# Kernel tuning notes

Hardware: AMD Instinct MI355X
Metric: run time of the kernel (lower is better)

The kernel has to match this reference:

```python
import jax, jax.numpy as jnp
import numpy as np

NUM_EXPERTS = 64
TOP_K = 2
TEMPERATURE = 1.0
MOMENTUM = 0.9


def _l2norm(x, axis=-1):
    # torch F.normalize: x / max(||x||, eps)
    n = jnp.linalg.norm(x, axis=axis, keepdims=True)
    return x / jnp.maximum(n, 1e-12)


def setup_inputs() -> dict:
    key = jax.random.key(0)
    k1, k2 = jax.random.split(key)
    hidden_states = jax.random.normal(k1, (4, 4096, 2048), dtype=jnp.float32)
    centers = _l2norm(jax.random.normal(k2, (NUM_EXPERTS, 2048), dtype=jnp.float32))
    return {"hidden_states": hidden_states, "centers": centers}


def reference(hidden_states, centers):
    B, T, H = hidden_states.shape
    flat = hidden_states.reshape(-1, H).astype(jnp.float32)  # [N, H]
    N = flat.shape[0]

    # cosine-similarity logits
    reps_n = _l2norm(flat)
    centers_n = _l2norm(centers)
    temp = jnp.maximum(jnp.float32(TEMPERATURE), 1e-6)
    logits = (reps_n @ centers_n.T) / temp  # [N, E]

    probs = jax.nn.softmax(logits, axis=-1)
    top_w, top_ids = jax.lax.top_k(probs, TOP_K)  # [N, k]
    top_w = top_w / (jnp.sum(top_w, axis=-1, keepdims=True) + 1e-9)

    # EMA center update from top-1 routed expert (training+update path)
    route = top_ids[:, 0]  # [N]
    sums = jax.ops.segment_sum(flat, route, num_segments=NUM_EXPERTS)  # [E, H]
    counts = jax.ops.segment_sum(jnp.ones((N, 1), jnp.float32), route,
                                 num_segments=NUM_EXPERTS)  # [E, 1]
    means = sums / (counts + 1e-6)
    updated = _l2norm(MOMENTUM * centers + (1.0 - MOMENTUM) * means)
    new_centers = jnp.where(counts > 0, updated, centers)

    top_ids = top_ids.reshape(B, T, TOP_K)
    top_w = top_w.reshape(B, T, TOP_K)
    return top_ids, top_w, new_centers
```

## Files before the change

kernel.cpp:

```cpp
#include <hip/hip_runtime.h>
#include <math.h>

#define NTOK 16384
#define HDIM 2048
#define NEXP 64
#define KK   32
#define TAU  5e-5f
#define MAXB 2048
#define TB   32
#define TPAD 36

typedef __attribute__((ext_vector_type(8))) short short8;
typedef __attribute__((ext_vector_type(4))) float f32x4;
typedef __attribute__((ext_vector_type(2))) unsigned int uint2v;


__global__ __launch_bounds__(256)
void zero_kernel(float* p, int n) {
  int i = blockIdx.x * 256 + threadIdx.x;
  if (i < n) p[i] = 0.0f;
}

__device__ __forceinline__ float block_reduce_sum(float v, float* red) {
  #pragma unroll
  for (int o = 32; o > 0; o >>= 1) v += __shfl_down(v, o, 64);
  int lane = threadIdx.x & 63;
  int wid  = threadIdx.x >> 6;
  if (lane == 0) red[wid] = v;
  __syncthreads();
  float s = red[0] + red[1] + red[2] + red[3];
  __syncthreads();
  return s;
}

__device__ __forceinline__ double block_reduce_sum_f64(double v, double* red) {
  const int tid = threadIdx.x;
  red[tid] = v;
  __syncthreads();
  if (tid < 128) red[tid] += red[tid + 128];
  __syncthreads();
  if (tid < 64)  red[tid] += red[tid + 64];
  __syncthreads();
  double s = 0.0;
  if (tid < 64) {
    s = red[tid];
    #pragma unroll
    for (int o = 32; o > 0; o >>= 1) s += __shfl_down(s, o, 64);
  }
  if (tid == 0) red[0] = s;
  __syncthreads();
  s = red[0];
  __syncthreads();
  return s;
}

__global__ __launch_bounds__(256)
void cnorm_kernel(const float* __restrict__ c, float* __restrict__ inv_nc) {
  __shared__ float red[4];
  int e = blockIdx.x;
  float ss = 0.f;
  #pragma unroll
  for (int j = 0; j < 8; ++j) {
    float v = c[e * HDIM + threadIdx.x + j * 256];
    ss += v * v;
  }
  float tot = block_reduce_sum(ss, red);
  if (threadIdx.x == 0) inv_nc[e] = 1.0f / fmaxf(sqrtf(tot), 1e-12f);
}

__global__ __launch_bounds__(256)
void cprep_kernel(const float* __restrict__ c, float* __restrict__ inv_nc,
                  float* __restrict__ bn, unsigned short* __restrict__ cbh,
                  unsigned short* __restrict__ cbl) {
  __shared__ float red[4];
  __shared__ double redd[256];
  __shared__ float s_nc;
  const int e = blockIdx.x;
  const int tid = threadIdx.x;
  const float* cr = c + (size_t)e * HDIM;
  float ss = 0.f;
  double acc = 0.0;
  #pragma unroll
  for (int j = 0; j < 8; ++j) {
    float v = cr[tid + j * 256];
    ss += v * v;
    double dv = (double)v;
    acc += dv * dv;
  }
  float tot = block_reduce_sum(ss, red);
  double cn = block_reduce_sum_f64(acc, redd);
  if (tid == 0) {
    inv_nc[e] = 1.0f / fmaxf(sqrtf(tot), 1e-12f);
    s_nc = (float)fmax(sqrt(cn), 1e-12);
  }
  __syncthreads();
  const double nc = (double)s_nc;
  #pragma unroll
  for (int j = 0; j < 8; ++j) {
    const int k = tid + j * 256;
    const float v = cr[k];
    bn[(size_t)e * HDIM + k] = (float)((double)v / nc);
    unsigned u = __float_as_uint(v);
    unsigned h = u & 0xffff0000u;
    float r = v - __uint_as_float(h);
    cbh[(size_t)e * HDIM + k] = (unsigned short)(u >> 16);
    cbl[(size_t)e * HDIM + k] = (unsigned short)(__float_as_uint(r) >> 16);
  }
}

__device__ __forceinline__ void cvt2(float v0, float v1, unsigned &hi, unsigned &lo) {
  unsigned u0 = __float_as_uint(v0);
  unsigned u1 = __float_as_uint(v1);
  unsigned h0 = u0 & 0xffff0000u;
  unsigned h1 = u1 & 0xffff0000u;
  float r0 = v0 - __uint_as_float(h0);
  float r1 = v1 - __uint_as_float(h1);
  hi = (u0 >> 16) | h1;
  lo = (__float_as_uint(r0) >> 16) | (__float_as_uint(r1) & 0xffff0000u);
}

__global__ __launch_bounds__(256)
void fused_kernel(const float* __restrict__ x,
                  const unsigned short* __restrict__ cbh,
                  const unsigned short* __restrict__ cbl,
                  const float* __restrict__ inv_nc,
                  float* __restrict__ out, int* __restrict__ route,
                  int* __restrict__ nflag, int* __restrict__ flags) {
  __shared__ __align__(16) unsigned short Ah[2][TB][32];
  __shared__ __align__(16) unsigned short Al[2][TB][32];
  __shared__ __align__(16) unsigned short Bh[2][NEXP][32];
  __shared__ __align__(16) unsigned short Bl[2][NEXP][32];
  __shared__ float lg[NEXP][TPAD];
  __shared__ float xn_lds[TB];
  __shared__ float snc[NEXP];

  const int tid  = threadIdx.x;
  const int t0   = blockIdx.x * TB;
  const int sr   = tid >> 3;
  const int sq   = (tid & 7) * 4;
  const int er   = tid >> 2;
  const int eq   = (tid & 3) * 8;
  const int lane = tid & 63;
  const int w    = tid >> 6;
  const int m16  = (w & 1) * 16;
  const int nh32 = (w >> 1) * 32;
  const int fr   = lane & 15;
  const int fk   = (lane >> 4) * 8;

  if (tid < NEXP) snc[tid] = inv_nc[tid];

  const float* xptr = x + (size_t)(t0 + sr) * HDIM + sq;
  const unsigned short* bhptr = cbh + (size_t)er * HDIM + eq;
  const unsigned short* blptr = cbl + (size_t)er * HDIM + eq;

  f32x4 xp;
  short8 bhp, blp;
  float nacc = 0.f;

  auto stage = [&](int b) {
    unsigned h01, l01, h23, l23;
    cvt2(xp.x, xp.y, h01, l01);
    cvt2(xp.z, xp.w, h23, l23);
    *(uint2v*)&Ah[b][sr][sq] = (uint2v){h01, h23};
    *(uint2v*)&Al[b][sr][sq] = (uint2v){l01, l23};
    nacc += xp.x*xp.x + xp.y*xp.y + xp.z*xp.z + xp.w*xp.w;
    *(short8*)&Bh[b][er][eq] = bhp;
    *(short8*)&Bl[b][er][eq] = blp;
  };

  xp  = *(const f32x4*)(xptr);
  bhp = *(const short8*)(bhptr);
  blp = *(const short8*)(blptr);
  stage(0);
  xp  = *(const f32x4*)(xptr + KK);
  bhp = *(const short8*)(bhptr + KK);
  blp = *(const short8*)(blptr + KK);
  __syncthreads();

  f32x4 acc0 = (f32x4){0.f, 0.f, 0.f, 0.f};
  f32x4 acc1 = (f32x4){0.f, 0.f, 0.f, 0.f};

  for (int it = 0; it < 64; ++it) {
    const int cur = it & 1;
    short8 ah  = *(const short8*)&Ah[cur][m16 + fr][fk];
    short8 al  = *(const short8*)&Al[cur][m16 + fr][fk];
    short8 bh0 = *(const short8*)&Bh[cur][nh32 + fr][fk];
    short8 bl0 = *(const short8*)&Bl[cur][nh32 + fr][fk];
    short8 bh1 = *(const short8*)&Bh[cur][nh32 + 16 + fr][fk];
    short8 bl1 = *(const short8*)&Bl[cur][nh32 + 16 + fr][fk];
    if (it < 63) {
      stage(cur ^ 1);
      if (it < 62) {
        const int off = (it + 2) * KK;
        xp  = *(const f32x4*)(xptr + off);
        bhp = *(const short8*)(bhptr + off);
        blp = *(const short8*)(blptr + off);
      }
    }
    acc0 = __builtin_amdgcn_mfma_f32_16x16x32_bf16(ah, bh0, acc0, 0, 0, 0);
    acc0 = __builtin_amdgcn_mfma_f32_16x16x32_bf16(ah, bl0, acc0, 0, 0, 0);
    acc0 = __builtin_amdgcn_mfma_f32_16x16x32_bf16(al, bh0, acc0, 0, 0, 0);
    acc1 = __builtin_amdgcn_mfma_f32_16x16x32_bf16(ah, bh1, acc1, 0, 0, 0);
    acc1 = __builtin_amdgcn_mfma_f32_16x16x32_bf16(ah, bl1, acc1, 0, 0, 0);
    acc1 = __builtin_amdgcn_mfma_f32_16x16x32_bf16(al, bh1, acc1, 0, 0, 0);
    __syncthreads();
  }

  float s = nacc;
  s += __shfl_xor(s, 1, 64);
  s += __shfl_xor(s, 2, 64);
  s += __shfl_xor(s, 4, 64);
  if ((tid & 7) == 0) xn_lds[sr] = s;

  const int tb = m16 + (lane >> 4) * 4;
  *(f32x4*)&lg[nh32 + fr][tb]      = acc0;
  *(f32x4*)&lg[nh32 + 16 + fr][tb] = acc1;
  __syncthreads();

  if (tid < TB) {
    const int t  = tid;
    const int tg = t0 + t;
    const float inv_nx = 1.0f / fmaxf(sqrtf(xn_lds[t]), 1e-12f);
    float m1 = -1e30f, m2 = -1e30f, m3 = -1e30f;
    int i1 = 0, i2 = 0;
    #pragma unroll
    for (int e = 0; e < NEXP; ++e) {
      float l = lg[e][t] * snc[e] * inv_nx;
      if (l > m1)      { m3 = m2; m2 = m1; i2 = i1; m1 = l; i1 = e; }
      else if (l > m2) { m3 = m2; m2 = l; i2 = e; }
      else if (l > m3) { m3 = l; }
    }
    float Z = 0.f;
    #pragma unroll
    for (int e = 0; e < NEXP; ++e)
      Z += expf(lg[e][t] * snc[e] * inv_nx - m1);
    const float p1w = 1.0f / Z;
    const float p2w = expf(m2 - m1) / Z;
    const float s2  = p1w + p2w + 1e-9f;
    out[tg * 2 + 0] = (float)i1;
    out[tg * 2 + 1] = (float)i2;
    out[2 * NTOK + tg * 2 + 0] = p1w / s2;
    out[2 * NTOK + tg * 2 + 1] = p2w / s2;
    route[tg] = i1;
    if ((m1 - m2) < TAU || (m2 - m3) < TAU) {
      int idx = atomicAdd(nflag, 1);
      flags[idx] = tg;
    }
  }
}

__global__ __launch_bounds__(256)
void refine_np_kernel(const float* __restrict__ x, const float* __restrict__ bn,
                      float* __restrict__ out, int* __restrict__ route,
                      const int* __restrict__ nflag, const int* __restrict__ flags) {
  __shared__ float a_lds[HDIM];
  __shared__ double redd[256];
  __shared__ float lf[NEXP];
  __shared__ float s_nx;
  const int tid  = threadIdx.x;
  const int lane = tid & 63;
  const int w    = tid >> 6;
  const int n = *nflag;
  for (int j = blockIdx.x; j < n; j += gridDim.x) {
    const int t = flags[j];
    const float* xr = x + (size_t)t * HDIM;
    double xacc = 0.0;
    #pragma unroll
    for (int i = 0; i < 8; ++i) {
      double v = (double)xr[tid + 256 * i];
      xacc += v * v;
    }
    double xn = block_reduce_sum_f64(xacc, redd);
    if (tid == 0) s_nx = (float)fmax(sqrt(xn), 1e-12);
    __syncthreads();
    const double nx = (double)s_nx;
    #pragma unroll
    for (int i = 0; i < 8; ++i) {
      int k = tid + 256 * i;
      a_lds[k] = (float)((double)xr[k] / nx);
    }
    __syncthreads();
    #pragma unroll 1
    for (int ei = 0; ei < 16; ++ei) {
      const int e = w * 16 + ei;
      const float* br = bn + (size_t)e * HDIM;
      double d = 0.0;
      #pragma unroll 8
      for (int i = 0; i < 32; ++i) {
        int k = lane + 64 * i;
        d += (double)a_lds[k] * (double)br[k];
      }
      #pragma unroll
      for (int o = 32; o > 0; o >>= 1) d += __shfl_down(d, o, 64);
      if (lane == 0) lf[e] = (float)d;
    }
    __syncthreads();
    if (tid == 0) {
      float m32 = lf[0];
      for (int ee = 1; ee < NEXP; ++ee) m32 = fmaxf(m32, lf[ee]);
      float ex[NEXP];
      for (int ee = 0; ee < NEXP; ++ee)
        ex[ee] = (float)exp((double)(lf[ee] - m32));
      float r[8];
      #pragma unroll
      for (int q = 0; q < 8; ++q) r[q] = ex[q];
      for (int i = 8; i < NEXP; i += 8)
        #pragma unroll
        for (int q = 0; q < 8; ++q) r[q] += ex[i + q];
      const float Z = ((r[0] + r[1]) + (r[2] + r[3])) + ((r[4] + r[5]) + (r[6] + r[7]));
      float p1 = -1.f, p2 = -1.f;
      int i1 = 0, i2 = 0;
      for (int ee = 0; ee < NEXP; ++ee) {
        float p = ex[ee] / Z;
        if (p > p1)      { p2 = p1; i2 = i1; p1 = p; i1 = ee; }
        else if (p > p2) { p2 = p; i2 = ee; }
      }
      const float s = (p1 + p2) + 1e-9f;
      out[t * 2 + 0] = (float)i1;
      out[t * 2 + 1] = (float)i2;
      out[2 * NTOK + t * 2 + 0] = p1 / s;
      out[2 * NTOK + t * 2 + 1] = p2 / s;
      route[t] = i1;
    }
    __syncthreads();
  }
}

__global__ __launch_bounds__(64)
void refine_np_slow(const float* __restrict__ x, const float* __restrict__ c,
                    float* __restrict__ out, int* __restrict__ route,
                    const int* __restrict__ nflag, const int* __restrict__ flags) {
  __shared__ float lf[NEXP];
  const int e = threadIdx.x;
  const int n = *nflag;
  for (int j = blockIdx.x; j < n; j += gridDim.x) {
    const int t = flags[j];
    const float* xr = x + (size_t)t * HDIM;
    const float* cr = c + (size_t)e * HDIM;
    double xn = 0.0, cn = 0.0;
    for (int k = 0; k < HDIM; ++k) {
      double xv = (double)xr[k];
      double cv = (double)cr[k];
      xn += xv * xv;
      cn += cv * cv;
    }
    const float nx32 = (float)fmax(sqrt(xn), 1e-12);
    const float nc32 = (float)fmax(sqrt(cn), 1e-12);
    double d = 0.0;
    for (int k = 0; k < HDIM; ++k) {
      float a = (float)((double)xr[k] / (double)nx32);
      float b = (float)((double)cr[k] / (double)nc32);
      d += (double)a * (double)b;
    }
    lf[e] = (float)d;
    __syncthreads();
    if (e == 0) {
      float m32 = lf[0];
      for (int ee = 1; ee < NEXP; ++ee) m32 = fmaxf(m32, lf[ee]);
      float ex[NEXP];
      for (int ee = 0; ee < NEXP; ++ee)
        ex[ee] = (float)exp((double)(lf[ee] - m32));
      float r[8];
      #pragma unroll
      for (int q = 0; q < 8; ++q) r[q] = ex[q];
      for (int i = 8; i < NEXP; i += 8)
        #pragma unroll
        for (int q = 0; q < 8; ++q) r[q] += ex[i + q];
      const float Z = ((r[0] + r[1]) + (r[2] + r[3])) + ((r[4] + r[5]) + (r[6] + r[7]));
      float p1 = -1.f, p2 = -1.f;
      int i1 = 0, i2 = 0;
      for (int ee = 0; ee < NEXP; ++ee) {
        float p = ex[ee] / Z;
        if (p > p1)      { p2 = p1; i2 = i1; p1 = p; i1 = ee; }
        else if (p > p2) { p2 = p; i2 = ee; }
      }
      const float s = (p1 + p2) + 1e-9f;
      out[t * 2 + 0] = (float)i1;
      out[t * 2 + 1] = (float)i2;
      out[2 * NTOK + t * 2 + 0] = p1 / s;
      out[2 * NTOK + t * 2 + 1] = p2 / s;
      route[t] = i1;
    }
    __syncthreads();
  }
}

__global__ __launch_bounds__(256)
void scatter_kernel(const int* __restrict__ route, int* __restrict__ cursor,
                    int* __restrict__ bucket) {
  const int t = blockIdx.x * 256 + threadIdx.x;
  const int e = route[t];
  const int pos = atomicAdd(&cursor[e], 1);
  if (pos < MAXB) bucket[e * MAXB + pos] = t;
}

__global__ __launch_bounds__(256)
void segsum_dense(const float* __restrict__ x, const int* __restrict__ cursor,
                  const int* __restrict__ bucket, float* __restrict__ sums) {
  __shared__ int ts[MAXB];
  const int e   = blockIdx.x >> 3;
  const int hc  = blockIdx.x & 7;
  const int hb  = hc * 256;
  const int tid = threadIdx.x;
  int n = cursor[e];
  if (n > MAXB) n = MAXB;
  for (int i = tid; i < n; i += 256) ts[i] = bucket[e * MAXB + i];
  __syncthreads();
  float a[8];
  #pragma unroll
  for (int q = 0; q < 8; ++q) a[q] = 0.f;
  int i = 0;
  for (; i + 7 < n; i += 8) {
    #pragma unroll
    for (int q = 0; q < 8; ++q)
      a[q] += x[(size_t)ts[i + q] * HDIM + hb + tid];
  }
  for (; i < n; ++i) a[0] += x[(size_t)ts[i] * HDIM + hb + tid];
  const float s = ((a[0] + a[1]) + (a[2] + a[3])) + ((a[4] + a[5]) + (a[6] + a[7]));
  sums[e * HDIM + hb + tid] = s;
}

__global__ __launch_bounds__(256)
void finalize_kernel(const float* __restrict__ c, const float* __restrict__ sums,
                     const int* __restrict__ counts, float* __restrict__ out) {
  __shared__ float red[4];
  const int e = blockIdx.x;
  const int tid = threadIdx.x;
  const float cnt = (float)counts[e];
  const float minv = 1.0f / (cnt + 1e-6f);
  float u[8], cv[8];
  float ss = 0.f;
  #pragma unroll
  for (int j = 0; j < 8; ++j) {
    int h = tid + j * 256;
    cv[j] = c[e * HDIM + h];
    float mean = sums[e * HDIM + h] * minv;
    u[j] = 0.9f * cv[j] + 0.1f * mean;
    ss += u[j] * u[j];
  }
  float tot = block_reduce_sum(ss, red);
  float sc = 1.0f / fmaxf(sqrtf(tot), 1e-12f);
  const bool nz = cnt > 0.f;
  #pragma unroll
  for (int j = 0; j < 8; ++j) {
    int h = tid + j * 256;
    out[4 * NTOK + e * HDIM + h] = nz ? u[j] * sc : cv[j];
  }
}

__global__ __launch_bounds__(256)
void router_kernel(const float* __restrict__ x, const float* __restrict__ c,
                   const float* __restrict__ inv_nc, float* __restrict__ out,
                   int* __restrict__ route, int* __restrict__ nflag,
                   int* __restrict__ flags) {
  __shared__ __align__(16) float xs[64][36];
  __shared__ float lgs[64][67];
  const int tid  = threadIdx.x;
  const int lane = tid & 63;
  const int w    = tid >> 6;
  const int t0   = blockIdx.x * 64;
  const int e0   = __builtin_amdgcn_readfirstlane(w * 16);
  const float* cb = c + (size_t)e0 * HDIM;
  const int st = tid >> 3;
  const int sk = (tid & 7) * 4;
  float acc[16];
  #pragma unroll
  for (int e = 0; e < 16; ++e) acc[e] = 0.f;
  float nacc = 0.f;
  float4 p0 = *(const float4*)&x[(size_t)(t0 + st)      * HDIM + sk];
  float4 p1 = *(const float4*)&x[(size_t)(t0 + st + 32) * HDIM + sk];
  for (int k0 = 0; k0 < HDIM; k0 += 32) {
    __syncthreads();
    *(float4*)&xs[st][sk]      = p0;
    *(float4*)&xs[st + 32][sk] = p1;
    __syncthreads();
    const int kn = k0 + 32;
    if (kn < HDIM) {
      p0 = *(const float4*)&x[(size_t)(t0 + st)      * HDIM + kn + sk];
      p1 = *(const float4*)&x[(size_t)(t0 + st + 32) * HDIM + kn + sk];
    }
    float a[32];
    #pragma unroll
    for (int j = 0; j < 32; j += 4) {
      float4 v = *(const float4*)&xs[lane][j];
      a[j] = v.x; a[j+1] = v.y; a[j+2] = v.z; a[j+3] = v.w;
    }
    if (w == 0) {
      #pragma unroll
      for (int j = 0; j < 32; ++j) nacc += a[j] * a[j];
    }
    #pragma unroll
    for (int e = 0; e < 16; ++e) {
      const float* br = cb + (size_t)e * HDIM + k0;
      #pragma unroll
      for (int j = 0; j < 32; j += 4) {
        float4 bv = *(const float4*)&br[j];
        acc[e] += a[j]*bv.x + a[j+1]*bv.y + a[j+2]*bv.z + a[j+3]*bv.w;
      }
    }
  }
  #pragma unroll
  for (int e = 0; e < 16; ++e) lgs[lane][e0 + e] = acc[e] * inv_nc[e0 + e];
  __syncthreads();
  if (w == 0) {
    const float inv_nx = 1.0f / fmaxf(sqrtf(nacc), 1e-12f);
    float m1 = -1e30f, m2 = -1e30f, m3 = -1e30f;
    int i1 = 0, i2 = 0;
    for (int e = 0; e < NEXP; ++e) {
      float l = lgs[lane][e] * inv_nx;
      if (l > m1)      { m3 = m2; m2 = m1; i2 = i1; m1 = l; i1 = e; }
      else if (l > m2) { m3 = m2; m2 = l; i2 = e; }
      else if (l > m3) { m3 = l; }
    }
    float Z = 0.f;
    for (int e = 0; e < NEXP; ++e) Z += expf(lgs[lane][e] * inv_nx - m1);
    const float p1w = 1.0f / Z;
    const float p2w = expf(m2 - m1) / Z;
    const float s   = p1w + p2w + 1e-9f;
    const int tg = t0 + lane;
    out[tg * 2 + 0] = (float)i1;
    out[tg * 2 + 1] = (float)i2;
    out[2 * NTOK + tg * 2 + 0] = p1w / s;
    out[2 * NTOK + tg * 2 + 1] = p2w / s;
    route[tg] = i1;
    if ((m1 - m2) < TAU || (m2 - m3) < TAU) {
      int idx = atomicAdd(nflag, 1);
      flags[idx] = tg;
    }
  }
}

__global__ __launch_bounds__(512)
void segsum_kernel(const float* __restrict__ x, const int* __restrict__ route,
                   float* __restrict__ sums, int* __restrict__ counts) {
  __shared__ float ls[NEXP * 256];
  __shared__ int lcnt[NEXP];
  const int tid  = threadIdx.x;
  const int lane = tid & 63;
  const int w    = tid >> 6;
  const int hc   = blockIdx.x & 7;
  const int tg   = blockIdx.x >> 3;
  const int hb   = hc * 256;
  #pragma unroll
  for (int i = 0; i < 32; ++i) ls[tid + i * 512] = 0.f;
  if (tid < NEXP) lcnt[tid] = 0;
  __syncthreads();
  const int tbase = tg * 512 + w * 64;
  #pragma unroll 4
  for (int i = 0; i < 64; ++i) {
    const int t = tbase + i;
    const int e = route[t];
    const float* xr = x + (size_t)t * HDIM + hb + lane;
    #pragma unroll
    for (int j = 0; j < 4; ++j)
      atomicAdd(&ls[e * 256 + lane + 64 * j], xr[64 * j]);
    if (hc == 0 && lane == 0) atomicAdd(&lcnt[e], 1);
  }
  __syncthreads();
  #pragma unroll
  for (int i = tid; i < NEXP * 256; i += 512) {
    const int e = i >> 8, h = i & 255;
    atomicAdd(&sums[e * HDIM + hb + h], ls[i]);
  }
  if (hc == 0 && tid < NEXP && lcnt[tid] > 0) atomicAdd(&counts[tid], lcnt[tid]);
}

extern "C" void kernel_launch(void* const* d_in, const int* in_sizes, int n_in,
                              void* d_out, int out_size, void* d_ws, size_t ws_size,
                              hipStream_t stream) {
  const float* x = (const float*)d_in[0];
  const float* c = (const float*)d_in[1];
  float* out = (float*)d_out;
  float* ws = (float*)d_ws;

  float* inv_nc = ws;
  int*   counts = (int*)(ws + 64);
  int*   nflag  = (int*)(ws + 128);
  int*   route  = (int*)(ws + 192);
  int*   flags  = (int*)(ws + 16576);
  float* sums   = ws + 32960;
  float* bn     = ws + 164032;
  unsigned short* cbh = (unsigned short*)(ws + 295104);
  unsigned short* cbl = (unsigned short*)(ws + 360640);
  int*   bucket = (int*)(ws + 426176);

  const size_t NEED = 557248ull * 4ull;
  if (ws_size >= NEED) {
    zero_kernel<<<1, 256, 0, stream>>>(ws + 64, 128);
    cprep_kernel<<<NEXP, 256, 0, stream>>>(c, inv_nc, bn, cbh, cbl);
    fused_kernel<<<NTOK / TB, 256, 0, stream>>>(x, cbh, cbl, inv_nc, out, route, nflag, flags);
    refine_np_kernel<<<512, 256, 0, stream>>>(x, bn, out, route, nflag, flags);
    scatter_kernel<<<64, 256, 0, stream>>>(route, counts, bucket);
    segsum_dense<<<512, 256, 0, stream>>>(x, counts, bucket, sums);
    finalize_kernel<<<NEXP, 256, 0, stream>>>(c, sums, counts, out);
  } else {
    zero_kernel<<<1, 256, 0, stream>>>(ws + 64, 128);
    zero_kernel<<<512, 256, 0, stream>>>(sums, 131072);
    cnorm_kernel<<<NEXP, 256, 0, stream>>>(c, inv_nc);
    router_kernel<<<NTOK / 64, 256, 0, stream>>>(x, c, inv_nc, out, route, nflag, flags);
    refine_np_slow<<<1024, 64, 0, stream>>>(x, c, out, route, nflag, flags);
    segsum_kernel<<<256, 512, 0, stream>>>(x, route, sums, counts);
    finalize_kernel<<<NEXP, 256, 0, stream>>>(c, sums, counts, out);
  }
}
```

Before: 314.6 us.

## Load GEMM operands directly to registers, split segment-sum across more blocks, fold zeroing

The fused router GEMM no longer stages x and center tiles through LDS with per-iteration barriers. Each wave now loads its MFMA fragments straight from global memory into a four-slot register ring, which removes the __syncthreads calls from the main loop. The segment sum is split four ways over token ranges and uses float4 loads across 2048 blocks, with partial sums added in a new finalize kernel; this raises parallelism but adds extra workspace traffic. Zeroing the counters moves into cprep, which drops one kernel launch.

```diff
diff --git a/kernel.cpp b/kernel.cpp
--- a/kernel.cpp
+++ b/kernel.cpp
@@ -12,7 +12,7 @@
 
 typedef __attribute__((ext_vector_type(8))) short short8;
 typedef __attribute__((ext_vector_type(4))) float f32x4;
-typedef __attribute__((ext_vector_type(2))) unsigned int uint2v;
+typedef __attribute__((ext_vector_type(4))) unsigned int uint4v;
 
 
 __global__ __launch_bounds__(256)
@@ -71,12 +71,13 @@
 __global__ __launch_bounds__(256)
 void cprep_kernel(const float* __restrict__ c, float* __restrict__ inv_nc,
                   float* __restrict__ bn, unsigned short* __restrict__ cbh,
-                  unsigned short* __restrict__ cbl) {
+                  unsigned short* __restrict__ cbl, int* __restrict__ zr) {
   __shared__ float red[4];
   __shared__ double redd[256];
   __shared__ float s_nc;
   const int e = blockIdx.x;
   const int tid = threadIdx.x;
+  if (e == 0 && tid < 128) zr[tid] = 0;
   const float* cr = c + (size_t)e * HDIM;
   float ss = 0.f;
   double acc = 0.0;
@@ -126,95 +127,91 @@
                   const float* __restrict__ inv_nc,
                   float* __restrict__ out, int* __restrict__ route,
                   int* __restrict__ nflag, int* __restrict__ flags) {
-  __shared__ __align__(16) unsigned short Ah[2][TB][32];
-  __shared__ __align__(16) unsigned short Al[2][TB][32];
-  __shared__ __align__(16) unsigned short Bh[2][NEXP][32];
-  __shared__ __align__(16) unsigned short Bl[2][NEXP][32];
   __shared__ float lg[NEXP][TPAD];
   __shared__ float xn_lds[TB];
   __shared__ float snc[NEXP];
 
   const int tid  = threadIdx.x;
   const int t0   = blockIdx.x * TB;
-  const int sr   = tid >> 3;
-  const int sq   = (tid & 7) * 4;
-  const int er   = tid >> 2;
-  const int eq   = (tid & 3) * 8;
   const int lane = tid & 63;
   const int w    = tid >> 6;
-  const int m16  = (w & 1) * 16;
-  const int nh32 = (w >> 1) * 32;
+  const int tt   = (w & 1) * 16;
+  const int eh   = (w >> 1) * 32;
   const int fr   = lane & 15;
   const int fk   = (lane >> 4) * 8;
 
   if (tid < NEXP) snc[tid] = inv_nc[tid];
 
-  const float* xptr = x + (size_t)(t0 + sr) * HDIM + sq;
-  const unsigned short* bhptr = cbh + (size_t)er * HDIM + eq;
-  const unsigned short* blptr = cbl + (size_t)er * HDIM + eq;
-
-  f32x4 xp;
-  short8 bhp, blp;
-  float nacc = 0.f;
-
-  auto stage = [&](int b) {
-    unsigned h01, l01, h23, l23;
-    cvt2(xp.x, xp.y, h01, l01);
-    cvt2(xp.z, xp.w, h23, l23);
-    *(uint2v*)&Ah[b][sr][sq] = (uint2v){h01, h23};
-    *(uint2v*)&Al[b][sr][sq] = (uint2v){l01, l23};
-    nacc += xp.x*xp.x + xp.y*xp.y + xp.z*xp.z + xp.w*xp.w;
-    *(short8*)&Bh[b][er][eq] = bhp;
-    *(short8*)&Bl[b][er][eq] = blp;
-  };
-
-  xp  = *(const f32x4*)(xptr);
-  bhp = *(const short8*)(bhptr);
-  blp = *(const short8*)(blptr);
-  stage(0);
-  xp  = *(const f32x4*)(xptr + KK);
-  bhp = *(const short8*)(bhptr + KK);
-  blp = *(const short8*)(blptr + KK);
-  __syncthreads();
+  const float*          xa  = x   + (size_t)(t0 + tt + fr) * HDIM + fk;
+  const unsigned short* b0h = cbh + (size_t)(eh + fr)      * HDIM + fk;
+  const unsigned short* b0l = cbl + (size_t)(eh + fr)      * HDIM + fk;
+  const unsigned short* b1h = cbh + (size_t)(eh + 16 + fr) * HDIM + fk;
+  const unsigned short* b1l = cbl + (size_t)(eh + 16 + fr) * HDIM + fk;
 
   f32x4 acc0 = (f32x4){0.f, 0.f, 0.f, 0.f};
   f32x4 acc1 = (f32x4){0.f, 0.f, 0.f, 0.f};
-
-  for (int it = 0; it < 64; ++it) {
-    const int cur = it & 1;
-    short8 ah  = *(const short8*)&Ah[cur][m16 + fr][fk];
-    short8 al  = *(const short8*)&Al[cur][m16 + fr][fk];
-    short8 bh0 = *(const short8*)&Bh[cur][nh32 + fr][fk];
-    short8 bl0 = *(const short8*)&Bl[cur][nh32 + fr][fk];
-    short8 bh1 = *(const short8*)&Bh[cur][nh32 + 16 + fr][fk];
-    short8 bl1 = *(const short8*)&Bl[cur][nh32 + 16 + fr][fk];
-    if (it < 63) {
-      stage(cur ^ 1);
-      if (it < 62) {
-        const int off = (it + 2) * KK;
-        xp  = *(const f32x4*)(xptr + off);
-        bhp = *(const short8*)(bhptr + off);
-        blp = *(const short8*)(blptr + off);
-      }
-    }
-    acc0 = __builtin_amdgcn_mfma_f32_16x16x32_bf16(ah, bh0, acc0, 0, 0, 0);
-    acc0 = __builtin_amdgcn_mfma_f32_16x16x32_bf16(ah, bl0, acc0, 0, 0, 0);
-    acc0 = __builtin_amdgcn_mfma_f32_16x16x32_bf16(al, bh0, acc0, 0, 0, 0);
-    acc1 = __builtin_amdgcn_mfma_f32_16x16x32_bf16(ah, bh1, acc1, 0, 0, 0);
-    acc1 = __builtin_amdgcn_mfma_f32_16x16x32_bf16(ah, bl1, acc1, 0, 0, 0);
-    acc1 = __builtin_amdgcn_mfma_f32_16x16x32_bf16(al, bh1, acc1, 0, 0, 0);
-    __syncthreads();
-  }
+  float nacc = 0.f;
+
+  union U { uint4v u; short8 s; };
+
+  f32x4  Aa0, Aa1, Ba0, Ba1, Ca0, Ca1, Da0, Da1;
+  short8 Ah0, Al0, Ah1, Al1;
+  short8 Bh0, Bl0, Bh1, Bl1;
+  short8 Ch0, Cl0, Ch1, Cl1;
+  short8 Dh0, Dl0, Dh1, Dl1;
+
+  #define LDSLOT(S, i) do { const int o_ = (i) * KK;                      \
+    S##a0 = *(const f32x4*)(xa + o_);                                     \
+    S##a1 = *(const f32x4*)(xa + o_ + 4);                                 \
+    S##h0 = *(const short8*)(b0h + o_);                                   \
+    S##l0 = *(const short8*)(b0l + o_);                                   \
+    S##h1 = *(const short8*)(b1h + o_);                                   \
+    S##l1 = *(const short8*)(b1l + o_); } while (0)
+
+  #define CONSUME(S) do {                                                 \
+    unsigned h01_, l01_, h23_, l23_, h45_, l45_, h67_, l67_;              \
+    cvt2(S##a0.x, S##a0.y, h01_, l01_);                                   \
+    cvt2(S##a0.z, S##a0.w, h23_, l23_);                                   \
+    cvt2(S##a1.x, S##a1.y, h45_, l45_);                                   \
+    cvt2(S##a1.z, S##a1.w, h67_, l67_);                                   \
+    U ah_; ah_.u = (uint4v){h01_, h23_, h45_, h67_};                      \
+    U al_; al_.u = (uint4v){l01_, l23_, l45_, l67_};                      \
+    nacc += S##a0.x*S##a0.x + S##a0.y*S##a0.y + S##a0.z*S##a0.z + S##a0.w*S##a0.w \
+          + S##a1.x*S##a1.x + S##a1.y*S##a1.y + S##a1.z*S##a1.z + S##a1.w*S##a1.w; \
+    acc0 = __builtin_amdgcn_mfma_f32_16x16x32_bf16(ah_.s, S##h0, acc0, 0, 0, 0); \
+    acc0 = __builtin_amdgcn_mfma_f32_16x16x32_bf16(ah_.s, S##l0, acc0, 0, 0, 0); \
+    acc0 = __builtin_amdgcn_mfma_f32_16x16x32_bf16(al_.s, S##h0, acc0, 0, 0, 0); \
+    acc1 = __builtin_amdgcn_mfma_f32_16x16x32_bf16(ah_.s, S##h1, acc1, 0, 0, 0); \
+    acc1 = __builtin_amdgcn_mfma_f32_16x16x32_bf16(ah_.s, S##l1, acc1, 0, 0, 0); \
+    acc1 = __builtin_amdgcn_mfma_f32_16x16x32_bf16(al_.s, S##h1, acc1, 0, 0, 0); \
+  } while (0)
+
+  LDSLOT(A, 0);
+  LDSLOT(B, 1);
+  LDSLOT(C, 2);
+
+  #pragma unroll 1
+  for (int it = 0; it < 64; it += 4) {
+    LDSLOT(D, it + 3);
+    CONSUME(A);
+    if (it + 4 < 64) LDSLOT(A, it + 4);
+    CONSUME(B);
+    if (it + 5 < 64) LDSLOT(B, it + 5);
+    CONSUME(C);
+    if (it + 6 < 64) LDSLOT(C, it + 6);
+    CONSUME(D);
+  }
+  #undef LDSLOT
+  #undef CONSUME
 
   float s = nacc;
-  s += __shfl_xor(s, 1, 64);
-  s += __shfl_xor(s, 2, 64);
-  s += __shfl_xor(s, 4, 64);
-  if ((tid & 7) == 0) xn_lds[sr] = s;
-
-  const int tb = m16 + (lane >> 4) * 4;
-  *(f32x4*)&lg[nh32 + fr][tb]      = acc0;
-  *(f32x4*)&lg[nh32 + 16 + fr][tb] = acc1;
+  s += __shfl_xor(s, 16, 64);
+  s += __shfl_xor(s, 32, 64);
+  if (lane < 16) xn_lds[tt + lane] = s;
+
+  const int tb = tt + (lane >> 4) * 4;
+  *(f32x4*)&lg[eh + fr][tb]      = acc0;
+  *(f32x4*)&lg[eh + 16 + fr][tb] = acc1;
   __syncthreads();
 
   if (tid < TB) {
@@ -395,29 +392,64 @@
 }
 
 __global__ __launch_bounds__(256)
-void segsum_dense(const float* __restrict__ x, const int* __restrict__ cursor,
-                  const int* __restrict__ bucket, float* __restrict__ sums) {
-  __shared__ int ts[MAXB];
-  const int e   = blockIdx.x >> 3;
-  const int hc  = blockIdx.x & 7;
+void segsum_part(const float* __restrict__ x, const int* __restrict__ cursor,
+                 const int* __restrict__ bucket, float* __restrict__ psum) {
+  __shared__ f32x4 part[4][64];
+  const int e   = blockIdx.x >> 5;
+  const int hc  = (blockIdx.x >> 2) & 7;
+  const int ts  = blockIdx.x & 3;
   const int hb  = hc * 256;
   const int tid = threadIdx.x;
+  const int rg  = tid >> 6;
+  const int cc  = tid & 63;
   int n = cursor[e];
   if (n > MAXB) n = MAXB;
-  for (int i = tid; i < n; i += 256) ts[i] = bucket[e * MAXB + i];
-  __syncthreads();
-  float a[8];
-  #pragma unroll
-  for (int q = 0; q < 8; ++q) a[q] = 0.f;
-  int i = 0;
-  for (; i + 7 < n; i += 8) {
-    #pragma unroll
-    for (int q = 0; q < 8; ++q)
-      a[q] += x[(size_t)ts[i + q] * HDIM + hb + tid];
-  }
-  for (; i < n; ++i) a[0] += x[(size_t)ts[i] * HDIM + hb + tid];
-  const float s = ((a[0] + a[1]) + (a[2] + a[3])) + ((a[4] + a[5]) + (a[6] + a[7]));
-  sums[e * HDIM + hb + tid] = s;
+  const int nq = (n + 3) >> 2;
+  const int lo = ts * nq;
+  const int hi = min(lo + nq, n);
+  const int* bk = bucket + e * MAXB;
+  f32x4 a = (f32x4){0.f, 0.f, 0.f, 0.f};
+  #pragma unroll 4
+  for (int i = lo + rg; i < hi; i += 4)
+    a += *(const f32x4*)(x + (size_t)bk[i] * HDIM + hb + cc * 4);
+  part[rg][cc] = a;
+  __syncthreads();
+  if (tid < 64) {
+    f32x4 s = part[0][tid] + part[1][tid] + part[2][tid] + part[3][tid];
+    *(f32x4*)&psum[(size_t)(ts * NEXP + e) * HDIM + hb + tid * 4] = s;
+  }
+}
+
+__global__ __launch_bounds__(256)
+void finalize4_kernel(const float* __restrict__ c, const float* __restrict__ psum,
+                      const int* __restrict__ counts, float* __restrict__ out) {
+  __shared__ float red[4];
+  const int e = blockIdx.x;
+  const int tid = threadIdx.x;
+  const float cnt = (float)counts[e];
+  const float minv = 1.0f / (cnt + 1e-6f);
+  float u[8], cv[8];
+  float ss = 0.f;
+  #pragma unroll
+  for (int j = 0; j < 8; ++j) {
+    int h = tid + j * 256;
+    cv[j] = c[e * HDIM + h];
+    float sm = psum[(size_t)(0 * NEXP + e) * HDIM + h]
+             + psum[(size_t)(1 * NEXP + e) * HDIM + h]
+             + psum[(size_t)(2 * NEXP + e) * HDIM + h]
+             + psum[(size_t)(3 * NEXP + e) * HDIM + h];
+    float mean = sm * minv;
+    u[j] = 0.9f * cv[j] + 0.1f * mean;
+    ss += u[j] * u[j];
+  }
+  float tot = block_reduce_sum(ss, red);
+  float sc = 1.0f / fmaxf(sqrtf(tot), 1e-12f);
+  const bool nz = cnt > 0.f;
+  #pragma unroll
+  for (int j = 0; j < 8; ++j) {
+    int h = tid + j * 256;
+    out[4 * NTOK + e * HDIM + h] = nz ? u[j] * sc : cv[j];
+  }
 }
 
 __global__ __launch_bounds__(256)
@@ -583,16 +615,16 @@
   unsigned short* cbh = (unsigned short*)(ws + 295104);
   unsigned short* cbl = (unsigned short*)(ws + 360640);
   int*   bucket = (int*)(ws + 426176);
-
-  const size_t NEED = 557248ull * 4ull;
+  float* psum   = ws + 557248;
+
+  const size_t NEED = 1081536ull * 4ull;
   if (ws_size >= NEED) {
-    zero_kernel<<<1, 256, 0, stream>>>(ws + 64, 128);
-    cprep_kernel<<<NEXP, 256, 0, stream>>>(c, inv_nc, bn, cbh, cbl);
+    cprep_kernel<<<NEXP, 256, 0, stream>>>(c, inv_nc, bn, cbh, cbl, counts);
     fused_kernel<<<NTOK / TB, 256, 0, stream>>>(x, cbh, cbl, inv_nc, out, route, nflag, flags);
     refine_np_kernel<<<512, 256, 0, stream>>>(x, bn, out, route, nflag, flags);
     scatter_kernel<<<64, 256, 0, stream>>>(route, counts, bucket);
-    segsum_dense<<<512, 256, 0, stream>>>(x, counts, bucket, sums);
-    finalize_kernel<<<NEXP, 256, 0, stream>>>(c, sums, counts, out);
+    segsum_part<<<2048, 256, 0, stream>>>(x, counts, bucket, psum);
+    finalize4_kernel<<<NEXP, 256, 0, stream>>>(c, psum, counts, out);
   } else {
     zero_kernel<<<1, 256, 0, stream>>>(ws + 64, 128);
     zero_kernel<<<512, 256, 0, stream>>>(sums, 131072);
```

New measurement: 346.3 us. 1.1x slower.
